# Kernel tuning notes

Measured on AMD Instinct MI355X. Metric: run time of the kernel, lower is better.

The kernel has to match this reference:

```python
import jax, jax.numpy as jnp
import numpy as np

B, C, H, W, R = 4, 64, 64, 64, 16  # batch, channels, height, width, reduced_channels
EPS = 1e-5


def setup_inputs() -> dict:
    key = jax.random.key(0)
    ks = jax.random.split(key, 10)
    s = 1.0 / np.sqrt(C)
    sf = 1.0 / np.sqrt(R)
    return {
        "x": jax.random.normal(ks[0], (B, C, H, W), jnp.float32),
        "y": jax.random.normal(ks[1], (B, C, H, W), jnp.float32),
        "Wq": jax.random.normal(ks[2], (R, C), jnp.float32) * s,
        "bq": jax.random.normal(ks[3], (R,), jnp.float32) * s,
        "Wk": jax.random.normal(ks[4], (R, C), jnp.float32) * s,
        "bk": jax.random.normal(ks[5], (R,), jnp.float32) * s,
        "Wv": jax.random.normal(ks[6], (R, C), jnp.float32) * s,
        "bv": jax.random.normal(ks[7], (R,), jnp.float32) * s,
        "Wf": jax.random.normal(ks[8], (C, R), jnp.float32) * sf,
        "bf": jax.random.normal(ks[9], (C,), jnp.float32) * sf,
        "ln_w": jnp.ones((C, H, W), jnp.float32),   # fresh nn.LayerNorm -> weight=1
        "ln_b": jnp.zeros((C, H, W), jnp.float32),  # fresh nn.LayerNorm -> bias=0
        "channels": C,
        "shape": H,
    }


def reference(x, y, Wq, bq, Wk, bk, Wv, bv, Wf, bf, ln_w, ln_b, channels, shape):
    b, c, h, w = x.shape
    xf = x.reshape(b, c, h * w)  # [B, C, N]
    yf = y.reshape(b, c, h * w)
    # 1x1 convs == per-pixel matmuls
    q = jnp.einsum('rc,bcn->brn', Wq, xf) + bq[None, :, None]   # [B, R, N]
    k = jnp.einsum('rc,bcn->brn', Wk, yf) + bk[None, :, None]
    v = jnp.einsum('rc,bcn->brn', Wv, yf) + bv[None, :, None]
    # unscaled attention: softmax(q^T k) over key axis
    attn = jax.nn.softmax(jnp.einsum('brn,brm->bnm', q, k), axis=-1)  # [B, N, N]
    out = jnp.einsum('brm,bnm->brn', v, attn)                          # [B, R, N]
    out = jnp.einsum('cr,brn->bcn', Wf, out) + bf[None, :, None]       # final 1x1 conv
    out = out.reshape(b, c, h, w) + x                                  # residual
    # LayerNorm over (C, H, W)
    mean = out.mean(axis=(1, 2, 3), keepdims=True)
    var = out.var(axis=(1, 2, 3), keepdims=True)
    out = (out - mean) * jax.lax.rsqrt(var + EPS) * ln_w + ln_b
    return out
```

## Files before the change

### kernel.cpp

```cpp
#include <hip/hip_runtime.h>
#include <hip/hip_bf16.h>
#include <math.h>

namespace {
constexpr int Bn = 4;
constexpr int Cn = 64;
constexpr int Nn = 4096;
constexpr int Rn = 16;
constexpr int Sn = 16;
constexpr int KPS = Nn / Sn;
constexpr int Tn = Nn / 16;
}

typedef __attribute__((ext_vector_type(4))) short v4s;
typedef __attribute__((ext_vector_type(4))) float v4f;

__device__ inline unsigned short f2bf(float f) {
    union { float f; unsigned u; } v; v.f = f;
    unsigned r = v.u + 0x7fffu + ((v.u >> 16) & 1u);
    return (unsigned short)(r >> 16);
}

__device__ inline unsigned pkbf(float a, float b) {
    __hip_bfloat162 t = __float22bfloat162_rn(make_float2(a, b));
    union { __hip_bfloat162 h; unsigned u; } v; v.h = t;
    return v.u;
}

__global__ __launch_bounds__(256) void qkv_proj(
    const float* __restrict__ x, const float* __restrict__ y,
    const float* __restrict__ Wq, const float* __restrict__ bq,
    const float* __restrict__ Wk, const float* __restrict__ bk,
    const float* __restrict__ Wv, const float* __restrict__ bv,
    unsigned short* __restrict__ q2, unsigned short* __restrict__ k2,
    unsigned short* __restrict__ v3, float* __restrict__ sums)
{
    if (blockIdx.x == 0 && threadIdx.x < 2 * Bn) sums[threadIdx.x] = 0.0f;

    const int job = blockIdx.x >> 8;
    const int rem = blockIdx.x & 255;
    const int b = rem >> 6;
    const int n = ((rem & 63) << 6) + (threadIdx.x & 63);
    const int rq = threadIdx.x >> 6;

    const float* sp = (job == 0 ? x : y) + (size_t)b * Cn * Nn + n;

    if (job == 0) {
        const float* wp = Wq + rq * 4 * Cn;
        float o0 = bq[rq*4+0], o1 = bq[rq*4+1], o2 = bq[rq*4+2], o3 = bq[rq*4+3];
#pragma unroll
        for (int c = 0; c < Cn; ++c) {
            const float xc = sp[(size_t)c * Nn];
            o0 += wp[c] * xc;
            o1 += wp[Cn + c] * xc;
            o2 += wp[2*Cn + c] * xc;
            o3 += wp[3*Cn + c] * xc;
        }
        unsigned short* dst = q2 + ((size_t)(b*Nn + n)) * Rn + rq*4;
        unsigned long long pk = (unsigned long long)pkbf(o0, o1)
                              | ((unsigned long long)pkbf(o2, o3) << 32);
        *(unsigned long long*)dst = pk;
    } else {
        const float* wk = Wk + rq * 4 * Cn;
        const float* wv = Wv + rq * 4 * Cn;
        float k0 = bk[rq*4+0], k1 = bk[rq*4+1], k2v = bk[rq*4+2], k3 = bk[rq*4+3];
        float u0 = bv[rq*4+0], u1 = bv[rq*4+1], u2 = bv[rq*4+2], u3 = bv[rq*4+3];
#pragma unroll
        for (int c = 0; c < Cn; ++c) {
            const float xc = sp[(size_t)c * Nn];
            k0 += wk[c] * xc;        k1 += wk[Cn + c] * xc;
            k2v += wk[2*Cn + c] * xc; k3 += wk[3*Cn + c] * xc;
            u0 += wv[c] * xc;        u1 += wv[Cn + c] * xc;
            u2 += wv[2*Cn + c] * xc; u3 += wv[3*Cn + c] * xc;
        }
        unsigned short* dk = k2 + ((size_t)(b*Nn + n)) * Rn + rq*4;
        unsigned long long pk = (unsigned long long)pkbf(k0, k1)
                              | ((unsigned long long)pkbf(k2v, k3) << 32);
        *(unsigned long long*)dk = pk;

        const int s  = n >> 8;
        const int kt = (n >> 4) & 15;
        const int ko = n & 15;
        unsigned short* vt = v3 + (((size_t)(b*Sn + s)*16 + kt) << 8)
                                + ((ko >> 2) << 6) + (ko & 3);
        vt[(rq*4+0)*4] = f2bf(u0);
        vt[(rq*4+1)*4] = f2bf(u1);
        vt[(rq*4+2)*4] = f2bf(u2);
        vt[(rq*4+3)*4] = f2bf(u3);
    }
}

__global__ __launch_bounds__(256) void attn_mfma(
    const unsigned short* __restrict__ q2, const unsigned short* __restrict__ k2,
    const unsigned short* __restrict__ v3,
    float* __restrict__ Pl, float* __restrict__ Pacc)
{
    const int lane = threadIdx.x & 63;
    const int wid  = threadIdx.x >> 6;
    const int bid  = blockIdx.x;
    const int b   = bid >> 8;
    const int rem = bid & 255;
    const int s   = rem >> 4;
    const int tbase = ((rem & 15) * 4 + wid) * 4;

    const int col = lane & 15;
    const int g4  = (lane >> 4) << 2;

    v4s qf[4];
#pragma unroll
    for (int i = 0; i < 4; ++i)
        qf[i] = *(const v4s*)(q2 + ((size_t)(b*Nn + (tbase+i)*16 + col)) * Rn + g4);

    const unsigned short* kp = k2 + ((size_t)(b*Nn + s*KPS) + col) * Rn + g4;
    const unsigned short* vtile = v3 + (((size_t)(b*Sn + s)) << 12);

    const v4f zf = {0.f, 0.f, 0.f, 0.f};
    v4f oacc[4] = {zf, zf, zf, zf};
    float l[4] = {0.f, 0.f, 0.f, 0.f};

#pragma unroll
    for (int kt = 0; kt < KPS/16; ++kt) {
        const v4s kf = *(const v4s*)(kp + kt * 16 * Rn);
        const v4s vf = *(const v4s*)(vtile + (kt << 8) + (lane << 2));

#pragma unroll
        for (int i = 0; i < 4; ++i) {
            v4f st = __builtin_amdgcn_mfma_f32_16x16x16bf16_1k(kf, qf[i], zf, 0, 0, 0);
            const float p0 = __expf(st[0]), p1 = __expf(st[1]);
            const float p2 = __expf(st[2]), p3 = __expf(st[3]);
            l[i] += (p0 + p1) + (p2 + p3);
            union { unsigned u[2]; v4s v; } uu;
            uu.u[0] = pkbf(p0, p1); uu.u[1] = pkbf(p2, p3);
            oacc[i] = __builtin_amdgcn_mfma_f32_16x16x16bf16_1k(vf, uu.v, oacc[i], 0, 0, 0);
        }
    }

#pragma unroll
    for (int i = 0; i < 4; ++i) {
        l[i] += __shfl_xor(l[i], 16);
        l[i] += __shfl_xor(l[i], 32);
    }
    if (lane < 16) {
#pragma unroll
        for (int i = 0; i < 4; ++i)
            Pl[(size_t)(b*Sn + s) * Nn + (tbase+i)*16 + lane] = l[i];
    }

#pragma unroll
    for (int i = 0; i < 4; ++i) {
        float4 a = make_float4(oacc[i][0], oacc[i][1], oacc[i][2], oacc[i][3]);
        *(float4*)(Pacc + ((size_t)((b*Tn + tbase+i)*Sn + s) * 64 + lane) * 4) = a;
    }
}

__global__ __launch_bounds__(256) void epilogue_fused(
    const float* __restrict__ Pacc, const float* __restrict__ Pl,
    const float* __restrict__ Wf, const float* __restrict__ bfb,
    const float* __restrict__ x,
    float* __restrict__ zout, float* __restrict__ sums)
{
    const int lane = threadIdx.x & 63;
    const int wid  = threadIdx.x >> 6;
    const int wv   = blockIdx.x * 4 + wid;
    const int b = wv >> 8;
    const int t = wv & 255;
    const int col = lane & 15;

    float4 acc = make_float4(0.f, 0.f, 0.f, 0.f);
#pragma unroll
    for (int s = 0; s < Sn; ++s) {
        const float4 p = *(const float4*)(Pacc + ((size_t)((b*Tn + t)*Sn + s) * 64 + lane) * 4);
        acc.x += p.x; acc.y += p.y; acc.z += p.z; acc.w += p.w;
    }

    float L = 0.f;
#pragma unroll
    for (int s = 0; s < Sn; ++s)
        L += Pl[(size_t)(b*Sn + s) * Nn + t*16 + col];
    const float invL = 1.f / L;

    float os[4] = {acc.x * invL, acc.y * invL, acc.z * invL, acc.w * invL};

    float orv[Rn];
#pragma unroll
    for (int k = 0; k < 4; ++k)
#pragma unroll
        for (int j = 0; j < 4; ++j)
            orv[k*4+j] = __shfl(os[j], col + 16*k);

    const int cg = lane >> 4;
    const int n = t*16 + col;
    const float* xp = x + (size_t)b * Cn * Nn + n;
    float* zp = zout + (size_t)b * Cn * Nn + n;

    float s1 = 0.f, s2 = 0.f;
#pragma unroll
    for (int cc = 0; cc < 16; ++cc) {
        const int c = cg * 16 + cc;
        const float4 w0 = *(const float4*)(Wf + c*Rn);
        const float4 w1 = *(const float4*)(Wf + c*Rn + 4);
        const float4 w2 = *(const float4*)(Wf + c*Rn + 8);
        const float4 w3 = *(const float4*)(Wf + c*Rn + 12);
        float z = bfb[c] + xp[(size_t)c * Nn];
        z += w0.x*orv[0]  + w0.y*orv[1]  + w0.z*orv[2]  + w0.w*orv[3];
        z += w1.x*orv[4]  + w1.y*orv[5]  + w1.z*orv[6]  + w1.w*orv[7];
        z += w2.x*orv[8]  + w2.y*orv[9]  + w2.z*orv[10] + w2.w*orv[11];
        z += w3.x*orv[12] + w3.y*orv[13] + w3.z*orv[14] + w3.w*orv[15];
        zp[(size_t)c * Nn] = z;
        s1 += z;
        s2 += z * z;
    }

#pragma unroll
    for (int off = 32; off > 0; off >>= 1) {
        s1 += __shfl_down(s1, off);
        s2 += __shfl_down(s2, off);
    }
    __shared__ float red[8];
    if ((threadIdx.x & 63) == 0) { red[wid] = s1; red[4 + wid] = s2; }
    __syncthreads();
    if (threadIdx.x == 0) {
        atomicAdd(&sums[2 * b + 0], red[0] + red[1] + red[2] + red[3]);
        atomicAdd(&sums[2 * b + 1], red[4] + red[5] + red[6] + red[7]);
    }
}

__global__ __launch_bounds__(256) void ln_apply(
    float* __restrict__ out, const float* __restrict__ lnw,
    const float* __restrict__ lnb, const float* __restrict__ sums)
{
    const int i = blockIdx.x * blockDim.x + threadIdx.x;
    const int b = i >> 16;
    const int jw = i & 65535;

    const float invM = 1.0f / (float)(Cn * Nn);
    const float S1 = sums[2 * b + 0];
    const float S2 = sums[2 * b + 1];
    const float mean = S1 * invM;
    const float var = fmaxf(S2 * invM - mean * mean, 0.0f);
    const float rs = rsqrtf(var + 1e-5f);

    float4 z = ((const float4*)out)[i];
    const float4 w = ((const float4*)lnw)[jw];
    const float4 bb = ((const float4*)lnb)[jw];
    z.x = (z.x - mean) * rs * w.x + bb.x;
    z.y = (z.y - mean) * rs * w.y + bb.y;
    z.z = (z.z - mean) * rs * w.z + bb.z;
    z.w = (z.w - mean) * rs * w.w + bb.w;
    ((float4*)out)[i] = z;
}

extern "C" void kernel_launch(void* const* d_in, const int* in_sizes, int n_in,
                              void* d_out, int out_size, void* d_ws, size_t ws_size,
                              hipStream_t stream) {
    const float* x   = (const float*)d_in[0];
    const float* y   = (const float*)d_in[1];
    const float* Wq  = (const float*)d_in[2];
    const float* bq  = (const float*)d_in[3];
    const float* Wk  = (const float*)d_in[4];
    const float* bk  = (const float*)d_in[5];
    const float* Wv  = (const float*)d_in[6];
    const float* bv  = (const float*)d_in[7];
    const float* Wf  = (const float*)d_in[8];
    const float* bfv = (const float*)d_in[9];
    const float* lnw = (const float*)d_in[10];
    const float* lnb = (const float*)d_in[11];
    float* out = (float*)d_out;

    char* p = (char*)d_ws;
    unsigned short* q2 = (unsigned short*)p; p += (size_t)Bn*Nn*Rn*2;
    unsigned short* k2 = (unsigned short*)p; p += (size_t)Bn*Nn*Rn*2;
    unsigned short* v3 = (unsigned short*)p; p += (size_t)Bn*Nn*Rn*2;
    float* Pl   = (float*)p; p += (size_t)Bn*Sn*Nn*4;
    float* Pacc = (float*)p; p += (size_t)Bn*Tn*Sn*64*4*4;
    float* sums = (float*)p;

    qkv_proj<<<512, 256, 0, stream>>>(x, y, Wq, bq, Wk, bk, Wv, bv, q2, k2, v3, sums);
    attn_mfma<<<Bn * Sn * (Tn/4) / 4, 256, 0, stream>>>(q2, k2, v3, Pl, Pacc);
    epilogue_fused<<<Bn * Tn / 4, 256, 0, stream>>>(Pacc, Pl, Wf, bfv, x, out, sums);
    ln_apply<<<(Bn * Cn * Nn / 4) / 256, 256, 0, stream>>>(out, lnw, lnb, sums);
}
```

Before: 135.6 us.

## Halve key splits, use exp2 with prescaled q, store bf16 partials, split epilogue

Attention now uses 8 key splits instead of 16, and each wave handles 2 query tiles instead of 4. This raises the number of waves and halves the partial-sum traffic. Q is prescaled by log2(e) so the inner loop can use the hardware exp2 instruction in place of __expf. Partial output accumulators are stored as bf16 instead of fp32, which halves their write and read volume but adds rounding error. The epilogue splits each tile's channels across two waves for more parallelism, at the cost of reducing the partials twice.

```diff
diff --git a/kernel.cpp b/kernel.cpp
--- a/kernel.cpp
+++ b/kernel.cpp
@@ -7,9 +7,10 @@
 constexpr int Cn = 64;
 constexpr int Nn = 4096;
 constexpr int Rn = 16;
-constexpr int Sn = 16;
+constexpr int Sn = 8;
 constexpr int KPS = Nn / Sn;
 constexpr int Tn = Nn / 16;
+constexpr float LOG2E = 1.44269504088896340736f;
 }
 
 typedef __attribute__((ext_vector_type(4))) short v4s;
@@ -25,6 +26,13 @@
     __hip_bfloat162 t = __float22bfloat162_rn(make_float2(a, b));
     union { __hip_bfloat162 h; unsigned u; } v; v.h = t;
     return v.u;
+}
+
+__device__ inline float bflo(unsigned u) {
+    union { unsigned u; float f; } v; v.u = u << 16; return v.f;
+}
+__device__ inline float bfhi(unsigned u) {
+    union { unsigned u; float f; } v; v.u = u & 0xffff0000u; return v.f;
 }
 
 __global__ __launch_bounds__(256) void qkv_proj(
@@ -56,6 +64,7 @@
             o2 += wp[2*Cn + c] * xc;
             o3 += wp[3*Cn + c] * xc;
         }
+        o0 *= LOG2E; o1 *= LOG2E; o2 *= LOG2E; o3 *= LOG2E;
         unsigned short* dst = q2 + ((size_t)(b*Nn + n)) * Rn + rq*4;
         unsigned long long pk = (unsigned long long)pkbf(o0, o1)
                               | ((unsigned long long)pkbf(o2, o3) << 32);
@@ -78,10 +87,9 @@
                               | ((unsigned long long)pkbf(k2v, k3) << 32);
         *(unsigned long long*)dk = pk;
 
-        const int s  = n >> 8;
-        const int kt = (n >> 4) & 15;
-        const int ko = n & 15;
-        unsigned short* vt = v3 + (((size_t)(b*Sn + s)*16 + kt) << 8)
+        const int ktg = n >> 4;
+        const int ko  = n & 15;
+        unsigned short* vt = v3 + (((size_t)(b*256 + ktg)) << 8)
                                 + ((ko >> 2) << 6) + (ko & 3);
         vt[(rq*4+0)*4] = f2bf(u0);
         vt[(rq*4+1)*4] = f2bf(u1);
@@ -93,68 +101,73 @@
 __global__ __launch_bounds__(256) void attn_mfma(
     const unsigned short* __restrict__ q2, const unsigned short* __restrict__ k2,
     const unsigned short* __restrict__ v3,
-    float* __restrict__ Pl, float* __restrict__ Pacc)
+    float* __restrict__ Pl, uint2* __restrict__ Pacc)
 {
     const int lane = threadIdx.x & 63;
     const int wid  = threadIdx.x >> 6;
     const int bid  = blockIdx.x;
     const int b   = bid >> 8;
     const int rem = bid & 255;
-    const int s   = rem >> 4;
-    const int tbase = ((rem & 15) * 4 + wid) * 4;
+    const int s   = rem >> 5;
+    const int pair = ((rem & 31) << 2) + wid;
+    const int t0 = pair * 2, t1 = t0 + 1;
 
     const int col = lane & 15;
     const int g4  = (lane >> 4) << 2;
 
-    v4s qf[4];
-#pragma unroll
-    for (int i = 0; i < 4; ++i)
-        qf[i] = *(const v4s*)(q2 + ((size_t)(b*Nn + (tbase+i)*16 + col)) * Rn + g4);
+    const v4s qf0 = *(const v4s*)(q2 + ((size_t)(b*Nn + t0*16 + col)) * Rn + g4);
+    const v4s qf1 = *(const v4s*)(q2 + ((size_t)(b*Nn + t1*16 + col)) * Rn + g4);
 
     const unsigned short* kp = k2 + ((size_t)(b*Nn + s*KPS) + col) * Rn + g4;
-    const unsigned short* vtile = v3 + (((size_t)(b*Sn + s)) << 12);
+    const unsigned short* vtile = v3 + (((size_t)(b*256 + s*32)) << 8);
 
     const v4f zf = {0.f, 0.f, 0.f, 0.f};
-    v4f oacc[4] = {zf, zf, zf, zf};
-    float l[4] = {0.f, 0.f, 0.f, 0.f};
-
-#pragma unroll
+    v4f oacc0 = zf, oacc1 = zf;
+    float l0 = 0.f, l1 = 0.f;
+
+#pragma unroll 8
     for (int kt = 0; kt < KPS/16; ++kt) {
         const v4s kf = *(const v4s*)(kp + kt * 16 * Rn);
         const v4s vf = *(const v4s*)(vtile + (kt << 8) + (lane << 2));
 
-#pragma unroll
-        for (int i = 0; i < 4; ++i) {
-            v4f st = __builtin_amdgcn_mfma_f32_16x16x16bf16_1k(kf, qf[i], zf, 0, 0, 0);
-            const float p0 = __expf(st[0]), p1 = __expf(st[1]);
-            const float p2 = __expf(st[2]), p3 = __expf(st[3]);
-            l[i] += (p0 + p1) + (p2 + p3);
-            union { unsigned u[2]; v4s v; } uu;
-            uu.u[0] = pkbf(p0, p1); uu.u[1] = pkbf(p2, p3);
-            oacc[i] = __builtin_amdgcn_mfma_f32_16x16x16bf16_1k(vf, uu.v, oacc[i], 0, 0, 0);
-        }
-    }
-
-#pragma unroll
-    for (int i = 0; i < 4; ++i) {
-        l[i] += __shfl_xor(l[i], 16);
-        l[i] += __shfl_xor(l[i], 32);
-    }
+        v4f st0 = __builtin_amdgcn_mfma_f32_16x16x16bf16_1k(kf, qf0, zf, 0, 0, 0);
+        v4f st1 = __builtin_amdgcn_mfma_f32_16x16x16bf16_1k(kf, qf1, zf, 0, 0, 0);
+
+        const float p00 = __builtin_amdgcn_exp2f(st0[0]);
+        const float p01 = __builtin_amdgcn_exp2f(st0[1]);
+        const float p02 = __builtin_amdgcn_exp2f(st0[2]);
+        const float p03 = __builtin_amdgcn_exp2f(st0[3]);
+        const float p10 = __builtin_amdgcn_exp2f(st1[0]);
+        const float p11 = __builtin_amdgcn_exp2f(st1[1]);
+        const float p12 = __builtin_amdgcn_exp2f(st1[2]);
+        const float p13 = __builtin_amdgcn_exp2f(st1[3]);
+        l0 += (p00 + p01) + (p02 + p03);
+        l1 += (p10 + p11) + (p12 + p13);
+
+        union { unsigned u[2]; v4s v; } u0, u1;
+        u0.u[0] = pkbf(p00, p01); u0.u[1] = pkbf(p02, p03);
+        u1.u[0] = pkbf(p10, p11); u1.u[1] = pkbf(p12, p13);
+
+        oacc0 = __builtin_amdgcn_mfma_f32_16x16x16bf16_1k(vf, u0.v, oacc0, 0, 0, 0);
+        oacc1 = __builtin_amdgcn_mfma_f32_16x16x16bf16_1k(vf, u1.v, oacc1, 0, 0, 0);
+    }
+
+    l0 += __shfl_xor(l0, 16); l0 += __shfl_xor(l0, 32);
+    l1 += __shfl_xor(l1, 16); l1 += __shfl_xor(l1, 32);
     if (lane < 16) {
-#pragma unroll
-        for (int i = 0; i < 4; ++i)
-            Pl[(size_t)(b*Sn + s) * Nn + (tbase+i)*16 + lane] = l[i];
-    }
-
-#pragma unroll
-    for (int i = 0; i < 4; ++i) {
-        float4 a = make_float4(oacc[i][0], oacc[i][1], oacc[i][2], oacc[i][3]);
-        *(float4*)(Pacc + ((size_t)((b*Tn + tbase+i)*Sn + s) * 64 + lane) * 4) = a;
-    }
+        Pl[(size_t)(b*Sn + s) * Nn + t0*16 + lane] = l0;
+        Pl[(size_t)(b*Sn + s) * Nn + t1*16 + lane] = l1;
+    }
+
+    uint2 a0, a1;
+    a0.x = pkbf(oacc0[0], oacc0[1]); a0.y = pkbf(oacc0[2], oacc0[3]);
+    a1.x = pkbf(oacc1[0], oacc1[1]); a1.y = pkbf(oacc1[2], oacc1[3]);
+    Pacc[(size_t)((b*Tn + t0)*Sn + s) * 64 + lane] = a0;
+    Pacc[(size_t)((b*Tn + t1)*Sn + s) * 64 + lane] = a1;
 }
 
 __global__ __launch_bounds__(256) void epilogue_fused(
-    const float* __restrict__ Pacc, const float* __restrict__ Pl,
+    const uint2* __restrict__ Pacc, const float* __restrict__ Pl,
     const float* __restrict__ Wf, const float* __restrict__ bfb,
     const float* __restrict__ x,
     float* __restrict__ zout, float* __restrict__ sums)
@@ -162,15 +175,17 @@
     const int lane = threadIdx.x & 63;
     const int wid  = threadIdx.x >> 6;
     const int wv   = blockIdx.x * 4 + wid;
-    const int b = wv >> 8;
-    const int t = wv & 255;
-    const int col = lane & 15;
-
-    float4 acc = make_float4(0.f, 0.f, 0.f, 0.f);
+    const int b    = wv >> 9;
+    const int t    = (wv >> 1) & 255;
+    const int half = wv & 1;
+    const int col  = lane & 15;
+
+    float a0 = 0.f, a1 = 0.f, a2 = 0.f, a3 = 0.f;
 #pragma unroll
     for (int s = 0; s < Sn; ++s) {
-        const float4 p = *(const float4*)(Pacc + ((size_t)((b*Tn + t)*Sn + s) * 64 + lane) * 4);
-        acc.x += p.x; acc.y += p.y; acc.z += p.z; acc.w += p.w;
+        const uint2 p = Pacc[(size_t)((b*Tn + t)*Sn + s) * 64 + lane];
+        a0 += bflo(p.x); a1 += bfhi(p.x);
+        a2 += bflo(p.y); a3 += bfhi(p.y);
     }
 
     float L = 0.f;
@@ -179,7 +194,7 @@
         L += Pl[(size_t)(b*Sn + s) * Nn + t*16 + col];
     const float invL = 1.f / L;
 
-    float os[4] = {acc.x * invL, acc.y * invL, acc.z * invL, acc.w * invL};
+    float os[4] = {a0 * invL, a1 * invL, a2 * invL, a3 * invL};
 
     float orv[Rn];
 #pragma unroll
@@ -195,8 +210,8 @@
 
     float s1 = 0.f, s2 = 0.f;
 #pragma unroll
-    for (int cc = 0; cc < 16; ++cc) {
-        const int c = cg * 16 + cc;
+    for (int cc = 0; cc < 8; ++cc) {
+        const int c = half*32 + cg*8 + cc;
         const float4 w0 = *(const float4*)(Wf + c*Rn);
         const float4 w1 = *(const float4*)(Wf + c*Rn + 4);
         const float4 w2 = *(const float4*)(Wf + c*Rn + 8);
@@ -272,11 +287,11 @@
     unsigned short* k2 = (unsigned short*)p; p += (size_t)Bn*Nn*Rn*2;
     unsigned short* v3 = (unsigned short*)p; p += (size_t)Bn*Nn*Rn*2;
     float* Pl   = (float*)p; p += (size_t)Bn*Sn*Nn*4;
-    float* Pacc = (float*)p; p += (size_t)Bn*Tn*Sn*64*4*4;
+    uint2* Pacc = (uint2*)p; p += (size_t)Bn*Tn*Sn*64*8;
     float* sums = (float*)p;
 
     qkv_proj<<<512, 256, 0, stream>>>(x, y, Wq, bq, Wk, bk, Wv, bv, q2, k2, v3, sums);
-    attn_mfma<<<Bn * Sn * (Tn/4) / 4, 256, 0, stream>>>(q2, k2, v3, Pl, Pacc);
-    epilogue_fused<<<Bn * Tn / 4, 256, 0, stream>>>(Pacc, Pl, Wf, bfv, x, out, sums);
+    attn_mfma<<<Bn * Sn * (Tn/2) / 4, 256, 0, stream>>>(q2, k2, v3, Pl, Pacc);
+    epilogue_fused<<<Bn * Tn * 2 / 4, 256, 0, stream>>>(Pacc, Pl, Wf, bfv, x, out, sums);
     ln_apply<<<(Bn * Cn * Nn / 4) / 256, 256, 0, stream>>>(out, lnw, lnb, sums);
 }
```

Measured after the change: 136.7 us. About the same (+0.9%).

## Fuse LayerNorm into epilogue via grid barrier, use exp2 and bf16 partials

Applied to the files above, without the earlier changes.

Merges the epilogue and LayerNorm apply kernels into one kernel. Each block keeps its outputs in registers and waits at a spin-wait grid barrier on an atomic counter until all blocks have added their per-batch sums. This removes the write and re-read of the full output tensor and one kernel launch. Q is pre-scaled by log2(e) so the attention kernel can use the hardware exp2. The partial attention accumulators are stored as bf16, which halves that intermediate traffic but loses precision. The barrier assumes all 512 blocks are resident at once and deadlocks if they are not.

```diff
diff --git a/kernel.cpp b/kernel.cpp
--- a/kernel.cpp
+++ b/kernel.cpp
@@ -10,6 +10,8 @@
 constexpr int Sn = 16;
 constexpr int KPS = Nn / Sn;
 constexpr int Tn = Nn / 16;
+constexpr float LOG2E = 1.44269504088896340736f;
+constexpr unsigned EPI_BLOCKS = 512;
 }
 
 typedef __attribute__((ext_vector_type(4))) short v4s;
@@ -25,6 +27,13 @@
     __hip_bfloat162 t = __float22bfloat162_rn(make_float2(a, b));
     union { __hip_bfloat162 h; unsigned u; } v; v.h = t;
     return v.u;
+}
+
+__device__ inline float bflo(unsigned u) {
+    union { unsigned u; float f; } v; v.u = u << 16; return v.f;
+}
+__device__ inline float bfhi(unsigned u) {
+    union { unsigned u; float f; } v; v.u = u & 0xffff0000u; return v.f;
 }
 
 __global__ __launch_bounds__(256) void qkv_proj(
@@ -33,9 +42,13 @@
     const float* __restrict__ Wk, const float* __restrict__ bk,
     const float* __restrict__ Wv, const float* __restrict__ bv,
     unsigned short* __restrict__ q2, unsigned short* __restrict__ k2,
-    unsigned short* __restrict__ v3, float* __restrict__ sums)
+    unsigned short* __restrict__ v3, float* __restrict__ sums,
+    unsigned* __restrict__ cnt)
 {
-    if (blockIdx.x == 0 && threadIdx.x < 2 * Bn) sums[threadIdx.x] = 0.0f;
+    if (blockIdx.x == 0) {
+        if (threadIdx.x < 2 * Bn) sums[threadIdx.x] = 0.0f;
+        if (threadIdx.x == 8) *cnt = 0u;
+    }
 
     const int job = blockIdx.x >> 8;
     const int rem = blockIdx.x & 255;
@@ -56,6 +69,7 @@
             o2 += wp[2*Cn + c] * xc;
             o3 += wp[3*Cn + c] * xc;
         }
+        o0 *= LOG2E; o1 *= LOG2E; o2 *= LOG2E; o3 *= LOG2E;
         unsigned short* dst = q2 + ((size_t)(b*Nn + n)) * Rn + rq*4;
         unsigned long long pk = (unsigned long long)pkbf(o0, o1)
                               | ((unsigned long long)pkbf(o2, o3) << 32);
@@ -78,10 +92,9 @@
                               | ((unsigned long long)pkbf(k2v, k3) << 32);
         *(unsigned long long*)dk = pk;
 
-        const int s  = n >> 8;
-        const int kt = (n >> 4) & 15;
-        const int ko = n & 15;
-        unsigned short* vt = v3 + (((size_t)(b*Sn + s)*16 + kt) << 8)
+        const int ktg = n >> 4;
+        const int ko  = n & 15;
+        unsigned short* vt = v3 + (((size_t)(b*256 + ktg)) << 8)
                                 + ((ko >> 2) << 6) + (ko & 3);
         vt[(rq*4+0)*4] = f2bf(u0);
         vt[(rq*4+1)*4] = f2bf(u1);
@@ -93,7 +106,7 @@
 __global__ __launch_bounds__(256) void attn_mfma(
     const unsigned short* __restrict__ q2, const unsigned short* __restrict__ k2,
     const unsigned short* __restrict__ v3,
-    float* __restrict__ Pl, float* __restrict__ Pacc)
+    float* __restrict__ Pl, uint2* __restrict__ Pacc)
 {
     const int lane = threadIdx.x & 63;
     const int wid  = threadIdx.x >> 6;
@@ -112,7 +125,7 @@
         qf[i] = *(const v4s*)(q2 + ((size_t)(b*Nn + (tbase+i)*16 + col)) * Rn + g4);
 
     const unsigned short* kp = k2 + ((size_t)(b*Nn + s*KPS) + col) * Rn + g4;
-    const unsigned short* vtile = v3 + (((size_t)(b*Sn + s)) << 12);
+    const unsigned short* vtile = v3 + (((size_t)(b*256 + s*16)) << 8);
 
     const v4f zf = {0.f, 0.f, 0.f, 0.f};
     v4f oacc[4] = {zf, zf, zf, zf};
@@ -126,8 +139,10 @@
 #pragma unroll
         for (int i = 0; i < 4; ++i) {
             v4f st = __builtin_amdgcn_mfma_f32_16x16x16bf16_1k(kf, qf[i], zf, 0, 0, 0);
-            const float p0 = __expf(st[0]), p1 = __expf(st[1]);
-            const float p2 = __expf(st[2]), p3 = __expf(st[3]);
+            const float p0 = __builtin_amdgcn_exp2f(st[0]);
+            const float p1 = __builtin_amdgcn_exp2f(st[1]);
+            const float p2 = __builtin_amdgcn_exp2f(st[2]);
+            const float p3 = __builtin_amdgcn_exp2f(st[3]);
             l[i] += (p0 + p1) + (p2 + p3);
             union { unsigned u[2]; v4s v; } uu;
             uu.u[0] = pkbf(p0, p1); uu.u[1] = pkbf(p2, p3);
@@ -148,29 +163,35 @@
 
 #pragma unroll
     for (int i = 0; i < 4; ++i) {
-        float4 a = make_float4(oacc[i][0], oacc[i][1], oacc[i][2], oacc[i][3]);
-        *(float4*)(Pacc + ((size_t)((b*Tn + tbase+i)*Sn + s) * 64 + lane) * 4) = a;
-    }
-}
-
-__global__ __launch_bounds__(256) void epilogue_fused(
-    const float* __restrict__ Pacc, const float* __restrict__ Pl,
+        uint2 a;
+        a.x = pkbf(oacc[i][0], oacc[i][1]);
+        a.y = pkbf(oacc[i][2], oacc[i][3]);
+        Pacc[(size_t)((b*Tn + tbase+i)*Sn + s) * 64 + lane] = a;
+    }
+}
+
+__global__ __launch_bounds__(256) void epilogue_ln(
+    const uint2* __restrict__ Pacc, const float* __restrict__ Pl,
     const float* __restrict__ Wf, const float* __restrict__ bfb,
     const float* __restrict__ x,
-    float* __restrict__ zout, float* __restrict__ sums)
+    const float* __restrict__ lnw, const float* __restrict__ lnb,
+    float* __restrict__ out, float* __restrict__ sums,
+    unsigned* __restrict__ cnt)
 {
     const int lane = threadIdx.x & 63;
     const int wid  = threadIdx.x >> 6;
     const int wv   = blockIdx.x * 4 + wid;
-    const int b = wv >> 8;
-    const int t = wv & 255;
-    const int col = lane & 15;
-
-    float4 acc = make_float4(0.f, 0.f, 0.f, 0.f);
+    const int b    = wv >> 9;
+    const int t    = (wv >> 1) & 255;
+    const int half = wv & 1;
+    const int col  = lane & 15;
+
+    float a0 = 0.f, a1 = 0.f, a2 = 0.f, a3 = 0.f;
 #pragma unroll
     for (int s = 0; s < Sn; ++s) {
-        const float4 p = *(const float4*)(Pacc + ((size_t)((b*Tn + t)*Sn + s) * 64 + lane) * 4);
-        acc.x += p.x; acc.y += p.y; acc.z += p.z; acc.w += p.w;
+        const uint2 p = Pacc[(size_t)((b*Tn + t)*Sn + s) * 64 + lane];
+        a0 += bflo(p.x); a1 += bfhi(p.x);
+        a2 += bflo(p.y); a3 += bfhi(p.y);
     }
 
     float L = 0.f;
@@ -179,7 +200,7 @@
         L += Pl[(size_t)(b*Sn + s) * Nn + t*16 + col];
     const float invL = 1.f / L;
 
-    float os[4] = {acc.x * invL, acc.y * invL, acc.z * invL, acc.w * invL};
+    float os[4] = {a0 * invL, a1 * invL, a2 * invL, a3 * invL};
 
     float orv[Rn];
 #pragma unroll
@@ -190,13 +211,14 @@
 
     const int cg = lane >> 4;
     const int n = t*16 + col;
+    const int c0 = half*32 + cg*8;
     const float* xp = x + (size_t)b * Cn * Nn + n;
-    float* zp = zout + (size_t)b * Cn * Nn + n;
-
+
+    float zreg[8];
     float s1 = 0.f, s2 = 0.f;
 #pragma unroll
-    for (int cc = 0; cc < 16; ++cc) {
-        const int c = cg * 16 + cc;
+    for (int cc = 0; cc < 8; ++cc) {
+        const int c = c0 + cc;
         const float4 w0 = *(const float4*)(Wf + c*Rn);
         const float4 w1 = *(const float4*)(Wf + c*Rn + 4);
         const float4 w2 = *(const float4*)(Wf + c*Rn + 8);
@@ -206,7 +228,7 @@
         z += w1.x*orv[4]  + w1.y*orv[5]  + w1.z*orv[6]  + w1.w*orv[7];
         z += w2.x*orv[8]  + w2.y*orv[9]  + w2.z*orv[10] + w2.w*orv[11];
         z += w3.x*orv[12] + w3.y*orv[13] + w3.z*orv[14] + w3.w*orv[15];
-        zp[(size_t)c * Nn] = z;
+        zreg[cc] = z;
         s1 += z;
         s2 += z * z;
     }
@@ -222,32 +244,31 @@
     if (threadIdx.x == 0) {
         atomicAdd(&sums[2 * b + 0], red[0] + red[1] + red[2] + red[3]);
         atomicAdd(&sums[2 * b + 1], red[4] + red[5] + red[6] + red[7]);
-    }
-}
-
-__global__ __launch_bounds__(256) void ln_apply(
-    float* __restrict__ out, const float* __restrict__ lnw,
-    const float* __restrict__ lnb, const float* __restrict__ sums)
-{
-    const int i = blockIdx.x * blockDim.x + threadIdx.x;
-    const int b = i >> 16;
-    const int jw = i & 65535;
+        __threadfence();
+        __hip_atomic_fetch_add(cnt, 1u, __ATOMIC_ACQ_REL, __HIP_MEMORY_SCOPE_AGENT);
+        while (__hip_atomic_load(cnt, __ATOMIC_ACQUIRE, __HIP_MEMORY_SCOPE_AGENT)
+               < EPI_BLOCKS) {
+            __builtin_amdgcn_s_sleep(8);
+        }
+        red[0] = __hip_atomic_load(&sums[2*b+0], __ATOMIC_RELAXED, __HIP_MEMORY_SCOPE_AGENT);
+        red[1] = __hip_atomic_load(&sums[2*b+1], __ATOMIC_RELAXED, __HIP_MEMORY_SCOPE_AGENT);
+    }
+    __syncthreads();
 
     const float invM = 1.0f / (float)(Cn * Nn);
-    const float S1 = sums[2 * b + 0];
-    const float S2 = sums[2 * b + 1];
-    const float mean = S1 * invM;
-    const float var = fmaxf(S2 * invM - mean * mean, 0.0f);
-    const float rs = rsqrtf(var + 1e-5f);
-
-    float4 z = ((const float4*)out)[i];
-    const float4 w = ((const float4*)lnw)[jw];
-    const float4 bb = ((const float4*)lnb)[jw];
-    z.x = (z.x - mean) * rs * w.x + bb.x;
-    z.y = (z.y - mean) * rs * w.y + bb.y;
-    z.z = (z.z - mean) * rs * w.z + bb.z;
-    z.w = (z.w - mean) * rs * w.w + bb.w;
-    ((float4*)out)[i] = z;
+    const float mean = red[0] * invM;
+    const float var  = fmaxf(red[1] * invM - mean * mean, 0.0f);
+    const float rs   = rsqrtf(var + 1e-5f);
+
+    const float* wp = lnw;
+    const float* bp = lnb;
+    float* op = out + (size_t)b * Cn * Nn + n;
+#pragma unroll
+    for (int cc = 0; cc < 8; ++cc) {
+        const int c = c0 + cc;
+        op[(size_t)c * Nn] = (zreg[cc] - mean) * rs * wp[(size_t)c * Nn + n]
+                           + bp[(size_t)c * Nn + n];
+    }
 }
 
 extern "C" void kernel_launch(void* const* d_in, const int* in_sizes, int n_in,
@@ -272,11 +293,13 @@
     unsigned short* k2 = (unsigned short*)p; p += (size_t)Bn*Nn*Rn*2;
     unsigned short* v3 = (unsigned short*)p; p += (size_t)Bn*Nn*Rn*2;
     float* Pl   = (float*)p; p += (size_t)Bn*Sn*Nn*4;
-    float* Pacc = (float*)p; p += (size_t)Bn*Tn*Sn*64*4*4;
-    float* sums = (float*)p;
-
-    qkv_proj<<<512, 256, 0, stream>>>(x, y, Wq, bq, Wk, bk, Wv, bv, q2, k2, v3, sums);
+    uint2* Pacc = (uint2*)p; p += (size_t)Bn*Tn*Sn*64*8;
+    float* sums = (float*)p; p += 8 * sizeof(float);
+    unsigned* cnt = (unsigned*)p;
+
+    qkv_proj<<<512, 256, 0, stream>>>(x, y, Wq, bq, Wk, bk, Wv, bv,
+                                      q2, k2, v3, sums, cnt);
     attn_mfma<<<Bn * Sn * (Tn/4) / 4, 256, 0, stream>>>(q2, k2, v3, Pl, Pacc);
-    epilogue_fused<<<Bn * Tn / 4, 256, 0, stream>>>(Pacc, Pl, Wf, bfv, x, out, sums);
-    ln_apply<<<(Bn * Cn * Nn / 4) / 256, 256, 0, stream>>>(out, lnw, lnb, sums);
-}
+    epilogue_ln<<<EPI_BLOCKS, 256, 0, stream>>>(Pacc, Pl, Wf, bfv, x,
+                                                lnw, lnb, out, sums, cnt);
+}
```

Result: slower. 166.7 us (+22.9%).

## Use exp2 with pre-scaled Q, store bf16 partial accumulators, split epilogue channels

Applied to the files above, without the earlier changes.

Q is pre-multiplied by log2(e) in the projection so the attention loop can call the hardware exp2 directly instead of __expf. The per-split output partials are stored as packed bf16 rather than fp32, halving the intermediate write and read traffic between attention and epilogue. The epilogue launches twice as many waves, each handling half the channels, to raise parallelism. The V layout indexing is rewritten equivalently. Rounding partial sums to bf16 and Q scaling in bf16 add precision error.

```diff
diff --git a/kernel.cpp b/kernel.cpp
--- a/kernel.cpp
+++ b/kernel.cpp
@@ -10,6 +10,7 @@
 constexpr int Sn = 16;
 constexpr int KPS = Nn / Sn;
 constexpr int Tn = Nn / 16;
+constexpr float LOG2E = 1.44269504088896340736f;
 }
 
 typedef __attribute__((ext_vector_type(4))) short v4s;
@@ -25,6 +26,13 @@
     __hip_bfloat162 t = __float22bfloat162_rn(make_float2(a, b));
     union { __hip_bfloat162 h; unsigned u; } v; v.h = t;
     return v.u;
+}
+
+__device__ inline float bflo(unsigned u) {
+    union { unsigned u; float f; } v; v.u = u << 16; return v.f;
+}
+__device__ inline float bfhi(unsigned u) {
+    union { unsigned u; float f; } v; v.u = u & 0xffff0000u; return v.f;
 }
 
 __global__ __launch_bounds__(256) void qkv_proj(
@@ -56,6 +64,7 @@
             o2 += wp[2*Cn + c] * xc;
             o3 += wp[3*Cn + c] * xc;
         }
+        o0 *= LOG2E; o1 *= LOG2E; o2 *= LOG2E; o3 *= LOG2E;
         unsigned short* dst = q2 + ((size_t)(b*Nn + n)) * Rn + rq*4;
         unsigned long long pk = (unsigned long long)pkbf(o0, o1)
                               | ((unsigned long long)pkbf(o2, o3) << 32);
@@ -78,10 +87,9 @@
                               | ((unsigned long long)pkbf(k2v, k3) << 32);
         *(unsigned long long*)dk = pk;
 
-        const int s  = n >> 8;
-        const int kt = (n >> 4) & 15;
-        const int ko = n & 15;
-        unsigned short* vt = v3 + (((size_t)(b*Sn + s)*16 + kt) << 8)
+        const int ktg = n >> 4;
+        const int ko  = n & 15;
+        unsigned short* vt = v3 + (((size_t)(b*256 + ktg)) << 8)
                                 + ((ko >> 2) << 6) + (ko & 3);
         vt[(rq*4+0)*4] = f2bf(u0);
         vt[(rq*4+1)*4] = f2bf(u1);
@@ -93,7 +101,7 @@
 __global__ __launch_bounds__(256) void attn_mfma(
     const unsigned short* __restrict__ q2, const unsigned short* __restrict__ k2,
     const unsigned short* __restrict__ v3,
-    float* __restrict__ Pl, float* __restrict__ Pacc)
+    float* __restrict__ Pl, uint2* __restrict__ Pacc)
 {
     const int lane = threadIdx.x & 63;
     const int wid  = threadIdx.x >> 6;
@@ -112,7 +120,7 @@
         qf[i] = *(const v4s*)(q2 + ((size_t)(b*Nn + (tbase+i)*16 + col)) * Rn + g4);
 
     const unsigned short* kp = k2 + ((size_t)(b*Nn + s*KPS) + col) * Rn + g4;
-    const unsigned short* vtile = v3 + (((size_t)(b*Sn + s)) << 12);
+    const unsigned short* vtile = v3 + (((size_t)(b*256 + s*16)) << 8);
 
     const v4f zf = {0.f, 0.f, 0.f, 0.f};
     v4f oacc[4] = {zf, zf, zf, zf};
@@ -126,8 +134,10 @@
 #pragma unroll
         for (int i = 0; i < 4; ++i) {
             v4f st = __builtin_amdgcn_mfma_f32_16x16x16bf16_1k(kf, qf[i], zf, 0, 0, 0);
-            const float p0 = __expf(st[0]), p1 = __expf(st[1]);
-            const float p2 = __expf(st[2]), p3 = __expf(st[3]);
+            const float p0 = __builtin_amdgcn_exp2f(st[0]);
+            const float p1 = __builtin_amdgcn_exp2f(st[1]);
+            const float p2 = __builtin_amdgcn_exp2f(st[2]);
+            const float p3 = __builtin_amdgcn_exp2f(st[3]);
             l[i] += (p0 + p1) + (p2 + p3);
             union { unsigned u[2]; v4s v; } uu;
             uu.u[0] = pkbf(p0, p1); uu.u[1] = pkbf(p2, p3);
@@ -148,13 +158,15 @@
 
 #pragma unroll
     for (int i = 0; i < 4; ++i) {
-        float4 a = make_float4(oacc[i][0], oacc[i][1], oacc[i][2], oacc[i][3]);
-        *(float4*)(Pacc + ((size_t)((b*Tn + tbase+i)*Sn + s) * 64 + lane) * 4) = a;
+        uint2 a;
+        a.x = pkbf(oacc[i][0], oacc[i][1]);
+        a.y = pkbf(oacc[i][2], oacc[i][3]);
+        Pacc[(size_t)((b*Tn + tbase+i)*Sn + s) * 64 + lane] = a;
     }
 }
 
 __global__ __launch_bounds__(256) void epilogue_fused(
-    const float* __restrict__ Pacc, const float* __restrict__ Pl,
+    const uint2* __restrict__ Pacc, const float* __restrict__ Pl,
     const float* __restrict__ Wf, const float* __restrict__ bfb,
     const float* __restrict__ x,
     float* __restrict__ zout, float* __restrict__ sums)
@@ -162,15 +174,17 @@
     const int lane = threadIdx.x & 63;
     const int wid  = threadIdx.x >> 6;
     const int wv   = blockIdx.x * 4 + wid;
-    const int b = wv >> 8;
-    const int t = wv & 255;
-    const int col = lane & 15;
-
-    float4 acc = make_float4(0.f, 0.f, 0.f, 0.f);
+    const int b    = wv >> 9;
+    const int t    = (wv >> 1) & 255;
+    const int half = wv & 1;
+    const int col  = lane & 15;
+
+    float a0 = 0.f, a1 = 0.f, a2 = 0.f, a3 = 0.f;
 #pragma unroll
     for (int s = 0; s < Sn; ++s) {
-        const float4 p = *(const float4*)(Pacc + ((size_t)((b*Tn + t)*Sn + s) * 64 + lane) * 4);
-        acc.x += p.x; acc.y += p.y; acc.z += p.z; acc.w += p.w;
+        const uint2 p = Pacc[(size_t)((b*Tn + t)*Sn + s) * 64 + lane];
+        a0 += bflo(p.x); a1 += bfhi(p.x);
+        a2 += bflo(p.y); a3 += bfhi(p.y);
     }
 
     float L = 0.f;
@@ -179,7 +193,7 @@
         L += Pl[(size_t)(b*Sn + s) * Nn + t*16 + col];
     const float invL = 1.f / L;
 
-    float os[4] = {acc.x * invL, acc.y * invL, acc.z * invL, acc.w * invL};
+    float os[4] = {a0 * invL, a1 * invL, a2 * invL, a3 * invL};
 
     float orv[Rn];
 #pragma unroll
@@ -190,13 +204,14 @@
 
     const int cg = lane >> 4;
     const int n = t*16 + col;
+    const int c0 = half*32 + cg*8;
     const float* xp = x + (size_t)b * Cn * Nn + n;
     float* zp = zout + (size_t)b * Cn * Nn + n;
 
     float s1 = 0.f, s2 = 0.f;
 #pragma unroll
-    for (int cc = 0; cc < 16; ++cc) {
-        const int c = cg * 16 + cc;
+    for (int cc = 0; cc < 8; ++cc) {
+        const int c = c0 + cc;
         const float4 w0 = *(const float4*)(Wf + c*Rn);
         const float4 w1 = *(const float4*)(Wf + c*Rn + 4);
         const float4 w2 = *(const float4*)(Wf + c*Rn + 8);
@@ -272,11 +287,12 @@
     unsigned short* k2 = (unsigned short*)p; p += (size_t)Bn*Nn*Rn*2;
     unsigned short* v3 = (unsigned short*)p; p += (size_t)Bn*Nn*Rn*2;
     float* Pl   = (float*)p; p += (size_t)Bn*Sn*Nn*4;
-    float* Pacc = (float*)p; p += (size_t)Bn*Tn*Sn*64*4*4;
+    uint2* Pacc = (uint2*)p; p += (size_t)Bn*Tn*Sn*64*8;
     float* sums = (float*)p;
 
-    qkv_proj<<<512, 256, 0, stream>>>(x, y, Wq, bq, Wk, bk, Wv, bv, q2, k2, v3, sums);
+    qkv_proj<<<512, 256, 0, stream>>>(x, y, Wq, bq, Wk, bk, Wv, bv,
+                                      q2, k2, v3, sums);
     attn_mfma<<<Bn * Sn * (Tn/4) / 4, 256, 0, stream>>>(q2, k2, v3, Pl, Pacc);
-    epilogue_fused<<<Bn * Tn / 4, 256, 0, stream>>>(Pacc, Pl, Wf, bfv, x, out, sums);
+    epilogue_fused<<<Bn * Tn * 2 / 4, 256, 0, stream>>>(Pacc, Pl, Wf, bfv, x, out, sums);
     ln_apply<<<(Bn * Cn * Nn / 4) / 256, 256, 0, stream>>>(out, lnw, lnb, sums);
 }
```

Result: slower. 138.8 us (+2.4%).
